# Kernel optimization log

Measured on AMD Instinct MI355X. Metric: run time of the kernel, lower is better.

Reference implementation:

```python
import jax, jax.numpy as jnp
import numpy as np

Y, Z, H, R = 32, 64, 256, 256  # y_dim, z_dim, h_dim, rnn_dim
T, B = 200, 2048


def setup_inputs() -> dict:
    key = jax.random.key(0)
    ks = jax.random.split(key, 32)
    w = lambda k, shape: jax.random.normal(k, shape, jnp.float32) * 0.05
    z32 = lambda n: jnp.zeros((n,), jnp.float32)
    return {
        "states": jax.random.normal(ks[0], (T, B, Y), jnp.float32),
        "eps": jax.random.normal(ks[1], (T - 1, B, Z), jnp.float32),
        # encoder q(z|x,y,h): Linear(2Y+R,H) ReLU Linear(H,H) ReLU
        "enc_w1": w(ks[2], (H, 2 * Y + R)), "enc_b1": z32(H),
        "enc_w2": w(ks[3], (H, H)), "enc_b2": z32(H),
        "enc_mw": w(ks[4], (Z, H)), "enc_mb": z32(Z),
        "enc_sw": w(ks[5], (Z, H)), "enc_sb": z32(Z),
        # prior p(z|y,h): Linear(Y+R,H) ReLU Linear(H,H) ReLU
        "pri_w1": w(ks[6], (H, Y + R)), "pri_b1": z32(H),
        "pri_w2": w(ks[7], (H, H)), "pri_b2": z32(H),
        "pri_mw": w(ks[8], (Z, H)), "pri_mb": z32(Z),
        "pri_sw": w(ks[9], (Z, H)), "pri_sb": z32(Z),
        # decoder p(x|y,z,h): Linear(Y+Z+R,H) ReLU Linear(H,H) ReLU
        "dec_w1": w(ks[10], (H, Y + Z + R)), "dec_b1": z32(H),
        "dec_w2": w(ks[11], (H, H)), "dec_b2": z32(H),
        "dec_mw": w(ks[12], (Y, H)), "dec_mb": z32(Y),
        "dec_sw": w(ks[13], (Y, H)), "dec_sb": z32(Y),
        # GRU(Y+Z -> R), 1 layer; torch gate order [r, z, n]
        "gru_wih": w(ks[14], (3 * R, Y + Z)), "gru_whh": w(ks[15], (3 * R, R)),
        "gru_bih": z32(3 * R), "gru_bhh": z32(3 * R),
    }


def reference(states, eps, enc_w1, enc_b1, enc_w2, enc_b2, enc_mw, enc_mb,
              enc_sw, enc_sb, pri_w1, pri_b1, pri_w2, pri_b2, pri_mw, pri_mb,
              pri_sw, pri_sb, dec_w1, dec_b1, dec_w2, dec_b2, dec_mw, dec_mb,
              dec_sw, dec_sb, gru_wih, gru_whh, gru_bih, gru_bhh):
    batch = states.shape[1]
    rnn_dim = gru_whh.shape[1]
    relu, sp = jax.nn.relu, jax.nn.softplus
    LOG2PI = jnp.float32(np.log(2.0 * np.pi))

    def mlp2(x, w1, b1, w2, b2):
        return relu(relu(x @ w1.T + b1) @ w2.T + b2)

    def step(h, inp):
        y, x, e = inp  # y=states[t], x=states[t+1], e: reparam noise
        enc_h = mlp2(jnp.concatenate([x, y, h], 1), enc_w1, enc_b1, enc_w2, enc_b2)
        em = enc_h @ enc_mw.T + enc_mb
        es = sp(enc_h @ enc_sw.T + enc_sb)
        pri_h = mlp2(jnp.concatenate([y, h], 1), pri_w1, pri_b1, pri_w2, pri_b2)
        pm = pri_h @ pri_mw.T + pri_mb
        ps = sp(pri_h @ pri_sw.T + pri_sb)
        z = em + es * e  # sample_gauss
        dec_h = mlp2(jnp.concatenate([y, z, h], 1), dec_w1, dec_b1, dec_w2, dec_b2)
        dm = dec_h @ dec_mw.T + dec_mb
        ds = sp(dec_h @ dec_sw.T + dec_sb)
        # GRU cell (torch gate order r,z,n)
        gi = jnp.concatenate([x, z], 1) @ gru_wih.T + gru_bih
        gh = h @ gru_whh.T + gru_bhh
        ir, iz, inn = jnp.split(gi, 3, axis=1)
        hr, hz, hn = jnp.split(gh, 3, axis=1)
        r = jax.nn.sigmoid(ir + hr)
        u = jax.nn.sigmoid(iz + hz)
        n = jnp.tanh(inn + r * hn)
        h_new = (1.0 - u) * n + u * h
        kl = 0.5 * jnp.sum(2.0 * jnp.log(ps / es) + (es ** 2 + (em - pm) ** 2) / ps ** 2 - 1.0)
        nll = jnp.sum(jnp.log(ds) + (x - dm) ** 2 / (2.0 * ds ** 2) + 0.5 * LOG2PI)
        return h_new, (kl, nll)

    h0 = jnp.zeros((batch, rnn_dim), states.dtype)
    _, (kls, nlls) = jax.lax.scan(step, h0, (states[:-1], states[1:], eps))
    # out = [kl_loss, recon_loss]
    return jnp.stack([jnp.sum(kls), jnp.sum(nlls)])
```

## Files before the change

### kernel.cpp

```cpp
#include <hip/hip_runtime.h>

typedef unsigned short u16;
typedef unsigned int u32;
typedef __bf16 bf16x8 __attribute__((ext_vector_type(8)));
typedef float f32x4 __attribute__((ext_vector_type(4)));

#define YD 32
#define ZD 64
#define HD 256
#define RD 256
#define TSTEPS 199
#define BB 2048
#define MROWS 32
#define NBLK 64
#define NTHR 1024
#define CATS 392
#define HBS  264
#define HES  136
#define HDS  72

enum : int {
  OFF_ENC_W1 = 0,
  OFF_ENC_W2 = 81920,
  OFF_ENC_H  = 147456,
  OFF_PRI_W1 = 180224,
  OFF_PRI_W2 = 253952,
  OFF_PRI_H  = 319488,
  OFF_DEC_W1 = 352256,
  OFF_DEC_W2 = 442368,
  OFF_DEC_H  = 507904,
  OFF_GWIH   = 524288,
  OFF_GWHH   = 598016,
};

__device__ __forceinline__ u16 f2bf(float f) {
  u32 u = __float_as_uint(f);
  u += 0x7fffu + ((u >> 16) & 1u);
  return (u16)(u >> 16);
}
__device__ __forceinline__ float bf2f(u16 b) {
  return __uint_as_float((u32)b << 16);
}
__device__ __forceinline__ float softplus_f(float x) {
  float l = __logf(1.f + __expf(-fabsf(x)));
  return x > 0.f ? x + l : l;
}
__device__ __forceinline__ float sigmoid_f(float x) {
  return __builtin_amdgcn_rcpf(1.f + __expf(-x));
}
__device__ __forceinline__ float tanh_f(float x) {
  float e = __expf(-2.f * fabsf(x));
  float t = (1.f - e) * __builtin_amdgcn_rcpf(1.f + e);
  return x >= 0.f ? t : -t;
}

template<int NT, int RT, int KS, int AS>
__device__ __forceinline__ void gemm_seg(f32x4 (&acc)[NT][RT],
    const u16* __restrict__ W, const int Kw, const int wrow0, const int wk0,
    const u16* A, const int acol0, const int rt0, const int lane)
{
  const int n = lane & 15, quad = lane >> 4;
  bf16x8 b[KS][NT];
  #pragma unroll
  for (int nt = 0; nt < NT; ++nt) {
    const u16* wp = W + (size_t)(wrow0 + nt * 16 + n) * Kw + wk0 + quad * 8;
    #pragma unroll
    for (int ks = 0; ks < KS; ++ks)
      b[ks][nt] = *reinterpret_cast<const bf16x8*>(wp + ks * 32);
  }
  #pragma unroll
  for (int ks = 0; ks < KS; ++ks) {
    bf16x8 a[RT];
    #pragma unroll
    for (int rt = 0; rt < RT; ++rt)
      a[rt] = *reinterpret_cast<const bf16x8*>(A + ((rt0 + rt) * 16 + n) * AS + acol0 + ks * 32 + quad * 8);
    #pragma unroll
    for (int nt = 0; nt < NT; ++nt)
      #pragma unroll
      for (int rt = 0; rt < RT; ++rt)
        acc[nt][rt] = __builtin_amdgcn_mfma_f32_16x16x32_bf16(a[rt], b[ks][nt], acc[nt][rt], 0, 0, 0);
  }
}

template<int RT, int DS>
__device__ __forceinline__ void store_relu(const f32x4 (&acc)[1][RT], u16* dst,
    const int col0, const int rt0, const float bias, const int lane)
{
  const int n = lane & 15, quad = lane >> 4;
  #pragma unroll
  for (int rt = 0; rt < RT; ++rt)
    #pragma unroll
    for (int i = 0; i < 4; ++i) {
      float v = fmaxf(acc[0][rt][i] + bias, 0.f);
      dst[((rt0 + rt) * 16 + quad * 4 + i) * DS + col0 + n] = f2bf(v);
    }
}

struct PrepArgs { const float* src[14]; int off[14]; int cnt[14]; };

__global__ void prep_weights(PrepArgs a, u16* __restrict__ dst) {
  const int j = blockIdx.y;
  const float* __restrict__ s = a.src[j];
  u16* d = dst + a.off[j];
  const int nel = a.cnt[j];
  for (int i = blockIdx.x * blockDim.x + threadIdx.x; i < nel; i += gridDim.x * blockDim.x)
    d[i] = f2bf(s[i]);
}

__global__ void zero_out_k(float* out) { if (threadIdx.x < 2) out[threadIdx.x] = 0.f; }

__global__ __launch_bounds__(NTHR, 4)
void vrnn_kernel(const float* __restrict__ states, const float* __restrict__ eps,
                 const float* __restrict__ enc_b1, const float* __restrict__ enc_b2,
                 const float* __restrict__ enc_mb, const float* __restrict__ enc_sb,
                 const float* __restrict__ pri_b1, const float* __restrict__ pri_b2,
                 const float* __restrict__ pri_mb, const float* __restrict__ pri_sb,
                 const float* __restrict__ dec_b1, const float* __restrict__ dec_b2,
                 const float* __restrict__ dec_mb, const float* __restrict__ dec_sb,
                 const float* __restrict__ gbih, const float* __restrict__ gbhh,
                 const u16* __restrict__ ws, float* __restrict__ out)
{
  __shared__ u16 cat[MROWS * CATS];
  __shared__ u16 hb1[MROWS * HBS];
  __shared__ u16 hb2[MROWS * HBS];
  __shared__ u16 hbhE[MROWS * HES];
  __shared__ u16 hbhP[MROWS * HES];
  __shared__ u16 hbhD[MROWS * HDS];

  const int tid = threadIdx.x;
  const int w = tid >> 6, lane = tid & 63;
  const int n = lane & 15, quad = lane >> 4;
  const int r0 = blockIdx.x * MROWS;
  const int n0 = w * 16;
  const int cgE = w & 7, rtE = w >> 3;
  const int cgD = w & 3, rtD = (w >> 2) & 1;

  const int jW = n0 + n;
  const float b1e = enc_b1[jW], b2e = enc_b2[jW];
  const float b1p = pri_b1[jW], b2p = pri_b2[jW];
  const float b1d = dec_b1[jW], b2d = dec_b2[jW];
  const float brg = gbih[jW] + gbhh[jW];
  const float bug = gbih[RD + jW] + gbhh[RD + jW];
  const float bing = gbih[2 * RD + jW];
  const float bhng = gbhh[2 * RD + jW];
  const float bhE = (cgE < 4) ? enc_mb[cgE * 16 + n] : enc_sb[(cgE - 4) * 16 + n];
  const float bhP = (cgE < 4) ? pri_mb[cgE * 16 + n] : pri_sb[(cgE - 4) * 16 + n];
  const float bhD = (cgD < 2) ? dec_mb[cgD * 16 + n] : dec_sb[(cgD - 2) * 16 + n];

  for (int i = tid; i < MROWS * (HD / 2); i += NTHR) {
    int row = i >> 7, c = (i & 127) * 2;
    *reinterpret_cast<u32*>(&cat[row * CATS + 128 + c]) = 0u;
  }

  float hreg[2][4];
  #pragma unroll
  for (int a = 0; a < 2; ++a)
    #pragma unroll
    for (int c = 0; c < 4; ++c) hreg[a][c] = 0.f;

  const int srow = (tid & 255) >> 3, sc4 = (tid & 7) * 4;
  float4 xyf = make_float4(0.f, 0.f, 0.f, 0.f);
  if (tid < 512)
    xyf = *reinterpret_cast<const float4*>(states + ((size_t)((tid < 256) ? 1 : 0) * BB + r0 + srow) * YD + sc4);

  const int mz = tid >> 5, jz = (tid & 31) * 2;
  const int mn = (tid & 511) >> 4, jn = (tid & 15) * 2;

  float kl_acc = 0.f, nll_acc = 0.f;

  for (int t = 0; t < TSTEPS; ++t) {
    if (tid < 512) {
      u16* d = cat + srow * CATS + ((tid < 256) ? 0 : 32) + sc4;
      d[0] = f2bf(xyf.x); d[1] = f2bf(xyf.y); d[2] = f2bf(xyf.z); d[3] = f2bf(xyf.w);
    }
    float2 ev2 = *reinterpret_cast<const float2*>(eps + ((size_t)t * BB + r0 + mz) * ZD + jz);
    float2 xs2 = make_float2(0.f, 0.f);
    if (tid < 512)
      xs2 = *reinterpret_cast<const float2*>(states + ((size_t)(t + 1) * BB + r0 + mn) * YD + jn);
    __syncthreads();

    {
      f32x4 acc[1][2] = {};
      gemm_seg<1, 2, 2, CATS>(acc, ws + OFF_ENC_W1, 320, n0, 0, cat, 0, 0, lane);
      gemm_seg<1, 2, 8, CATS>(acc, ws + OFF_ENC_W1, 320, n0, 64, cat, 128, 0, lane);
      store_relu<2, HBS>(acc, hb1, n0, 0, b1e, lane);
    }
    __syncthreads();

    {
      f32x4 acc[1][2] = {};
      gemm_seg<1, 2, 8, HBS>(acc, ws + OFF_ENC_W2, 256, n0, 0, hb1, 0, 0, lane);
      store_relu<2, HBS>(acc, hb2, n0, 0, b2e, lane);
    }
    __syncthreads();

    {
      f32x4 acc[1][1] = {};
      gemm_seg<1, 1, 8, HBS>(acc, ws + OFF_ENC_H, 256, cgE * 16, 0, hb2, 0, rtE, lane);
      #pragma unroll
      for (int i = 0; i < 4; ++i) {
        float v = acc[0][0][i] + bhE;
        if (cgE >= 4) v = softplus_f(v);
        hbhE[(rtE * 16 + quad * 4 + i) * HES + cgE * 16 + n] = f2bf(v);
      }
    }
    __syncthreads();

    {
      float em0 = bf2f(hbhE[mz * HES + jz]);
      float em1 = bf2f(hbhE[mz * HES + jz + 1]);
      float es0 = bf2f(hbhE[mz * HES + 64 + jz]);
      float es1 = bf2f(hbhE[mz * HES + 64 + jz + 1]);
      cat[mz * CATS + 64 + jz] = f2bf(em0 + es0 * ev2.x);
      cat[mz * CATS + 64 + jz + 1] = f2bf(em1 + es1 * ev2.y);
      f32x4 acc[1][2] = {};
      gemm_seg<1, 2, 1, CATS>(acc, ws + OFF_PRI_W1, 288, n0, 0, cat, 32, 0, lane);
      gemm_seg<1, 2, 8, CATS>(acc, ws + OFF_PRI_W1, 288, n0, 32, cat, 128, 0, lane);
      store_relu<2, HBS>(acc, hb1, n0, 0, b1p, lane);
    }
    __syncthreads();

    {
      f32x4 acc[1][2] = {};
      gemm_seg<1, 2, 8, HBS>(acc, ws + OFF_PRI_W2, 256, n0, 0, hb1, 0, 0, lane);
      store_relu<2, HBS>(acc, hb2, n0, 0, b2p, lane);
    }
    __syncthreads();

    {
      f32x4 acc[1][1] = {};
      gemm_seg<1, 1, 8, HBS>(acc, ws + OFF_PRI_H, 256, cgE * 16, 0, hb2, 0, rtE, lane);
      #pragma unroll
      for (int i = 0; i < 4; ++i) {
        float v = acc[0][0][i] + bhP;
        if (cgE >= 4) v = softplus_f(v);
        hbhP[(rtE * 16 + quad * 4 + i) * HES + cgE * 16 + n] = f2bf(v);
      }
    }
    __syncthreads();

    {
      #pragma unroll
      for (int c = 0; c < 2; ++c) {
        float em = bf2f(hbhE[mz * HES + jz + c]);
        float es = bf2f(hbhE[mz * HES + 64 + jz + c]);
        float pm = bf2f(hbhP[mz * HES + jz + c]);
        float ps = bf2f(hbhP[mz * HES + 64 + jz + c]);
        float d = em - pm;
        kl_acc += 0.5f * (2.f * __logf(ps * __builtin_amdgcn_rcpf(es))
                          + (es * es + d * d) / (ps * ps) - 1.f);
      }
      f32x4 acc[1][2] = {};
      gemm_seg<1, 2, 3, CATS>(acc, ws + OFF_DEC_W1, 352, n0, 0, cat, 32, 0, lane);
      gemm_seg<1, 2, 8, CATS>(acc, ws + OFF_DEC_W1, 352, n0, 96, cat, 128, 0, lane);
      store_relu<2, HBS>(acc, hb1, n0, 0, b1d, lane);
    }
    __syncthreads();

    {
      f32x4 acc[1][2] = {};
      gemm_seg<1, 2, 8, HBS>(acc, ws + OFF_DEC_W2, 256, n0, 0, hb1, 0, 0, lane);
      store_relu<2, HBS>(acc, hb2, n0, 0, b2d, lane);
    }
    __syncthreads();

    {
      if (w < 8) {
        f32x4 acc[1][1] = {};
        gemm_seg<1, 1, 8, HBS>(acc, ws + OFF_DEC_H, 256, cgD * 16, 0, hb2, 0, rtD, lane);
        #pragma unroll
        for (int i = 0; i < 4; ++i) {
          float v = acc[0][0][i] + bhD;
          if (cgD >= 2) v = softplus_f(v);
          hbhD[(rtD * 16 + quad * 4 + i) * HDS + cgD * 16 + n] = f2bf(v);
        }
      }
      f32x4 aH[1][2] = {};
      gemm_seg<1, 2, 8, CATS>(aH, ws + OFF_GWHH, 256, 2 * RD + n0, 0, cat, 128, 0, lane);
      {
        f32x4 aR[1][2] = {};
        gemm_seg<1, 2, 1, CATS>(aR, ws + OFF_GWIH, 96, n0, 0, cat, 0, 0, lane);
        gemm_seg<1, 2, 2, CATS>(aR, ws + OFF_GWIH, 96, n0, 32, cat, 64, 0, lane);
        gemm_seg<1, 2, 8, CATS>(aR, ws + OFF_GWHH, 256, n0, 0, cat, 128, 0, lane);
        #pragma unroll
        for (int rt = 0; rt < 2; ++rt)
          #pragma unroll
          for (int i = 0; i < 4; ++i)
            aH[0][rt][i] = sigmoid_f(aR[0][rt][i] + brg) * (aH[0][rt][i] + bhng);
      }
      {
        f32x4 aN[1][2] = {};
        gemm_seg<1, 2, 1, CATS>(aN, ws + OFF_GWIH, 96, 2 * RD + n0, 0, cat, 0, 0, lane);
        gemm_seg<1, 2, 2, CATS>(aN, ws + OFF_GWIH, 96, 2 * RD + n0, 32, cat, 64, 0, lane);
        #pragma unroll
        for (int rt = 0; rt < 2; ++rt)
          #pragma unroll
          for (int i = 0; i < 4; ++i)
            aH[0][rt][i] = tanh_f(aN[0][rt][i] + bing + aH[0][rt][i]);
      }
      {
        f32x4 aU[1][2] = {};
        gemm_seg<1, 2, 1, CATS>(aU, ws + OFF_GWIH, 96, RD + n0, 0, cat, 0, 0, lane);
        gemm_seg<1, 2, 2, CATS>(aU, ws + OFF_GWIH, 96, RD + n0, 32, cat, 64, 0, lane);
        gemm_seg<1, 2, 8, CATS>(aU, ws + OFF_GWHH, 256, RD + n0, 0, cat, 128, 0, lane);
        #pragma unroll
        for (int rt = 0; rt < 2; ++rt)
          #pragma unroll
          for (int i = 0; i < 4; ++i) {
            float u = sigmoid_f(aU[0][rt][i] + bug);
            hreg[rt][i] = (1.f - u) * aH[0][rt][i] + u * hreg[rt][i];
          }
      }
      const int tn = (t + 1 < TSTEPS) ? t + 1 : TSTEPS - 1;
      if (tid < 512)
        xyf = *reinterpret_cast<const float4*>(states + ((size_t)((tid < 256) ? tn + 1 : tn) * BB + r0 + srow) * YD + sc4);
    }
    __syncthreads();

    if (tid < 512) {
      #pragma unroll
      for (int c = 0; c < 2; ++c) {
        float dm = bf2f(hbhD[mn * HDS + jn + c]);
        float ds = bf2f(hbhD[mn * HDS + 32 + jn + c]);
        float xv = (c == 0) ? xs2.x : xs2.y;
        float dd = xv - dm;
        nll_acc += __logf(ds) + dd * dd / (2.f * ds * ds) + 0.91893853320467274178f;
      }
    }
    #pragma unroll
    for (int rt = 0; rt < 2; ++rt)
      #pragma unroll
      for (int i = 0; i < 4; ++i)
        cat[(rt * 16 + quad * 4 + i) * CATS + 128 + n0 + n] = f2bf(hreg[rt][i]);
  }

  float kv = kl_acc, nv = nll_acc;
  #pragma unroll
  for (int off = 32; off > 0; off >>= 1) {
    kv += __shfl_down(kv, off, 64);
    nv += __shfl_down(nv, off, 64);
  }
  if (lane == 0) {
    atomicAdd(out + 0, kv);
    atomicAdd(out + 1, nv);
  }
}

extern "C" void kernel_launch(void* const* d_in, const int* in_sizes, int n_in,
                              void* d_out, int out_size, void* d_ws, size_t ws_size,
                              hipStream_t stream) {
  const float* states = (const float*)d_in[0];
  const float* eps    = (const float*)d_in[1];
  u16* ws   = (u16*)d_ws;
  float* out = (float*)d_out;

  PrepArgs pa;
  const int jsrc[14] = {2, 4, 6, 8, 10, 12, 14, 16, 18, 20, 22, 24, 26, 27};
  const int joff[14] = {OFF_ENC_W1, OFF_ENC_W2, OFF_ENC_H, OFF_ENC_H + 16384,
                        OFF_PRI_W1, OFF_PRI_W2, OFF_PRI_H, OFF_PRI_H + 16384,
                        OFF_DEC_W1, OFF_DEC_W2, OFF_DEC_H, OFF_DEC_H + 8192,
                        OFF_GWIH, OFF_GWHH};
  const int jcnt[14] = {81920, 65536, 16384, 16384,
                        73728, 65536, 16384, 16384,
                        90112, 65536, 8192, 8192,
                        73728, 196608};
  for (int j = 0; j < 14; ++j) {
    pa.src[j] = (const float*)d_in[jsrc[j]];
    pa.off[j] = joff[j];
    pa.cnt[j] = jcnt[j];
  }

  zero_out_k<<<dim3(1), dim3(64), 0, stream>>>(out);
  prep_weights<<<dim3(64, 14), dim3(256), 0, stream>>>(pa, ws);
  vrnn_kernel<<<dim3(NBLK), dim3(NTHR), 0, stream>>>(
      states, eps,
      (const float*)d_in[3],  (const float*)d_in[5],
      (const float*)d_in[7],  (const float*)d_in[9],
      (const float*)d_in[11], (const float*)d_in[13],
      (const float*)d_in[15], (const float*)d_in[17],
      (const float*)d_in[19], (const float*)d_in[21],
      (const float*)d_in[23], (const float*)d_in[25],
      (const float*)d_in[28], (const float*)d_in[29],
      ws, out);
}
```

Measured before the change: 10.76 ms.

## Software-pipeline VRNN step: run encoder/GRU alongside prior/decoder of previous step

Restructures the per-step schedule so warp groups specialise. Warps 0-7 run the encoder and GRU for step t, warps 8-11 run the prior and warps 12-15 the decoder for step t-1, using double-buffered h, z and encoder-head buffers plus a triple-buffered y ring. This cuts the barriers per step from about ten to four and lets independent branches overlap. The batch tile per block is halved to 16 rows (128 blocks), which gives more blocks but less weight reuse per block, and the staggered index logic across t and t-1 risks off-by-one mistakes.

```diff
diff --git a/kernel.cpp b/kernel.cpp
--- a/kernel.cpp
+++ b/kernel.cpp
@@ -11,13 +11,15 @@
 #define RD 256
 #define TSTEPS 199
 #define BB 2048
-#define MROWS 32
-#define NBLK 64
+#define MROWS 16
+#define NBLK 128
 #define NTHR 1024
-#define CATS 392
-#define HBS  264
-#define HES  136
-#define HDS  72
+#define YS  40
+#define ZS  72
+#define HS  264
+#define HBS 264
+#define HES 136
+#define HDS 72
 
 enum : int {
   OFF_ENC_W1 = 0,
@@ -82,17 +84,17 @@
   }
 }
 
-template<int RT, int DS>
-__device__ __forceinline__ void store_relu(const f32x4 (&acc)[1][RT], u16* dst,
-    const int col0, const int rt0, const float bias, const int lane)
+template<int NT, int DS>
+__device__ __forceinline__ void store_relu_n(const f32x4 (&acc)[NT][1], u16* dst,
+    const int col0, const float (&bias)[NT], const int lane)
 {
   const int n = lane & 15, quad = lane >> 4;
   #pragma unroll
-  for (int rt = 0; rt < RT; ++rt)
+  for (int nt = 0; nt < NT; ++nt)
     #pragma unroll
     for (int i = 0; i < 4; ++i) {
-      float v = fmaxf(acc[0][rt][i] + bias, 0.f);
-      dst[((rt0 + rt) * 16 + quad * 4 + i) * DS + col0 + n] = f2bf(v);
+      float v = fmaxf(acc[nt][0][i] + bias[nt], 0.f);
+      dst[(quad * 4 + i) * DS + col0 + nt * 16 + n] = f2bf(v);
     }
 }
 
@@ -120,218 +122,261 @@
                  const float* __restrict__ gbih, const float* __restrict__ gbhh,
                  const u16* __restrict__ ws, float* __restrict__ out)
 {
-  __shared__ u16 cat[MROWS * CATS];
-  __shared__ u16 hb1[MROWS * HBS];
-  __shared__ u16 hb2[MROWS * HBS];
-  __shared__ u16 hbhE[MROWS * HES];
-  __shared__ u16 hbhP[MROWS * HES];
-  __shared__ u16 hbhD[MROWS * HDS];
+  __shared__ __align__(16) u16 yb[3][MROWS * YS];
+  __shared__ __align__(16) u16 zb[2][MROWS * ZS];
+  __shared__ __align__(16) u16 hbuf[2][MROWS * HS];
+  __shared__ __align__(16) u16 hb1A[MROWS * HBS], hb2A[MROWS * HBS];
+  __shared__ __align__(16) u16 hb1P[MROWS * HBS], hb2P[MROWS * HBS];
+  __shared__ __align__(16) u16 hb1D[MROWS * HBS], hb2D[MROWS * HBS];
+  __shared__ __align__(16) u16 hbhE[2][MROWS * HES];
+  __shared__ __align__(16) u16 hbhP[MROWS * HES];
+  __shared__ __align__(16) u16 hbhD[MROWS * HDS];
 
   const int tid = threadIdx.x;
   const int w = tid >> 6, lane = tid & 63;
   const int n = lane & 15, quad = lane >> 4;
   const int r0 = blockIdx.x * MROWS;
-  const int n0 = w * 16;
-  const int cgE = w & 7, rtE = w >> 3;
-  const int cgD = w & 3, rtD = (w >> 2) & 1;
-
-  const int jW = n0 + n;
-  const float b1e = enc_b1[jW], b2e = enc_b2[jW];
-  const float b1p = pri_b1[jW], b2p = pri_b2[jW];
-  const float b1d = dec_b1[jW], b2d = dec_b2[jW];
-  const float brg = gbih[jW] + gbhh[jW];
-  const float bug = gbih[RD + jW] + gbhh[RD + jW];
-  const float bing = gbih[2 * RD + jW];
-  const float bhng = gbhh[2 * RD + jW];
-  const float bhE = (cgE < 4) ? enc_mb[cgE * 16 + n] : enc_sb[(cgE - 4) * 16 + n];
-  const float bhP = (cgE < 4) ? pri_mb[cgE * 16 + n] : pri_sb[(cgE - 4) * 16 + n];
-  const float bhD = (cgD < 2) ? dec_mb[cgD * 16 + n] : dec_sb[(cgD - 2) * 16 + n];
+  const int n0A = w * 32;
+
+  float b1e[2] = {}, b2e[2] = {}, brg[2] = {}, bug[2] = {}, bing[2] = {}, bhng[2] = {};
+  float mbE = 0.f, sbE = 0.f;
+  float b1p[4] = {}, b2p[4] = {}, bhP[2] = {};
+  float b1d[4] = {}, b2d[4] = {}, bhD = 0.f;
+  if (w < 8) {
+    #pragma unroll
+    for (int s = 0; s < 2; ++s) {
+      const int c = n0A + s * 16 + n;
+      b1e[s] = enc_b1[c]; b2e[s] = enc_b2[c];
+      brg[s] = gbih[c] + gbhh[c];
+      bug[s] = gbih[RD + c] + gbhh[RD + c];
+      bing[s] = gbih[2 * RD + c];
+      bhng[s] = gbhh[2 * RD + c];
+    }
+    if (w < 4) { mbE = enc_mb[w * 16 + n]; sbE = enc_sb[w * 16 + n]; }
+  } else if (w < 12) {
+    const int p = w - 8;
+    #pragma unroll
+    for (int k = 0; k < 4; ++k) {
+      const int c = p * 64 + k * 16 + n;
+      b1p[k] = pri_b1[c]; b2p[k] = pri_b2[c];
+    }
+    #pragma unroll
+    for (int k = 0; k < 2; ++k) {
+      const int r = p * 32 + k * 16 + n;
+      bhP[k] = (r < 64) ? pri_mb[r] : pri_sb[r - 64];
+    }
+  } else {
+    const int d_ = w - 12;
+    #pragma unroll
+    for (int k = 0; k < 4; ++k) {
+      const int c = d_ * 64 + k * 16 + n;
+      b1d[k] = dec_b1[c]; b2d[k] = dec_b2[c];
+    }
+    const int r = d_ * 16 + n;
+    bhD = (r < 32) ? dec_mb[r] : dec_sb[r - 32];
+  }
 
   for (int i = tid; i < MROWS * (HD / 2); i += NTHR) {
     int row = i >> 7, c = (i & 127) * 2;
-    *reinterpret_cast<u32*>(&cat[row * CATS + 128 + c]) = 0u;
-  }
+    *reinterpret_cast<u32*>(&hbuf[0][row * HS + c]) = 0u;
+  }
+  if (tid < 256) {
+    const int row = tid >> 4, c2 = (tid & 15) * 2;
+    float2 a0 = *reinterpret_cast<const float2*>(states + ((size_t)0 * BB + r0 + row) * YD + c2);
+    float2 a1 = *reinterpret_cast<const float2*>(states + ((size_t)1 * BB + r0 + row) * YD + c2);
+    yb[0][row * YS + c2] = f2bf(a0.x); yb[0][row * YS + c2 + 1] = f2bf(a0.y);
+    yb[1][row * YS + c2] = f2bf(a1.x); yb[1][row * YS + c2 + 1] = f2bf(a1.y);
+  }
+  __syncthreads();
 
   float hreg[2][4];
   #pragma unroll
-  for (int a = 0; a < 2; ++a)
-    #pragma unroll
-    for (int c = 0; c < 4; ++c) hreg[a][c] = 0.f;
-
-  const int srow = (tid & 255) >> 3, sc4 = (tid & 7) * 4;
-  float4 xyf = make_float4(0.f, 0.f, 0.f, 0.f);
-  if (tid < 512)
-    xyf = *reinterpret_cast<const float4*>(states + ((size_t)((tid < 256) ? 1 : 0) * BB + r0 + srow) * YD + sc4);
-
-  const int mz = tid >> 5, jz = (tid & 31) * 2;
-  const int mn = (tid & 511) >> 4, jn = (tid & 15) * 2;
+  for (int s = 0; s < 2; ++s)
+    #pragma unroll
+    for (int i = 0; i < 4; ++i) hreg[s][i] = 0.f;
 
   float kl_acc = 0.f, nll_acc = 0.f;
-
-  for (int t = 0; t < TSTEPS; ++t) {
-    if (tid < 512) {
-      u16* d = cat + srow * CATS + ((tid < 256) ? 0 : 32) + sc4;
-      d[0] = f2bf(xyf.x); d[1] = f2bf(xyf.y); d[2] = f2bf(xyf.z); d[3] = f2bf(xyf.w);
-    }
-    float2 ev2 = *reinterpret_cast<const float2*>(eps + ((size_t)t * BB + r0 + mz) * ZD + jz);
-    float2 xs2 = make_float2(0.f, 0.f);
-    if (tid < 512)
-      xs2 = *reinterpret_cast<const float2*>(states + ((size_t)(t + 1) * BB + r0 + mn) * YD + jn);
+  int ym0 = 0, ym1 = 1, ym2 = 2;
+
+  for (int t = 0; t <= TSTEPS; ++t) {
+    const int pa = t & 1, pb = pa ^ 1;
+    f32x4 agh[3][2][1] = {};
+
+    if (w < 8) {
+      if (t < TSTEPS) {
+        f32x4 acc[2][1] = {};
+        gemm_seg<2,1,1,YS>(acc, ws + OFF_ENC_W1, 320, n0A, 0,   yb[ym1], 0, 0, lane);
+        gemm_seg<2,1,1,YS>(acc, ws + OFF_ENC_W1, 320, n0A, 32,  yb[ym0], 0, 0, lane);
+        gemm_seg<2,1,4,HS>(acc, ws + OFF_ENC_W1, 320, n0A, 64,  hbuf[pa], 0,   0, lane);
+        gemm_seg<2,1,4,HS>(acc, ws + OFF_ENC_W1, 320, n0A, 192, hbuf[pa], 128, 0, lane);
+        store_relu_n<2, HBS>(acc, hb1A, n0A, b1e, lane);
+        gemm_seg<2,1,4,HS>(agh[0], ws + OFF_GWHH, 256, n0A, 0,   hbuf[pa], 0,   0, lane);
+        gemm_seg<2,1,4,HS>(agh[0], ws + OFF_GWHH, 256, n0A, 128, hbuf[pa], 128, 0, lane);
+      }
+    } else if (w < 12) {
+      if (t > 0) {
+        const int n0 = (w - 8) * 64;
+        f32x4 acc[4][1] = {};
+        gemm_seg<4,1,1,YS>(acc, ws + OFF_PRI_W1, 288, n0, 0,   yb[ym2], 0, 0, lane);
+        gemm_seg<4,1,4,HS>(acc, ws + OFF_PRI_W1, 288, n0, 32,  hbuf[pb], 0,   0, lane);
+        gemm_seg<4,1,4,HS>(acc, ws + OFF_PRI_W1, 288, n0, 160, hbuf[pb], 128, 0, lane);
+        store_relu_n<4, HBS>(acc, hb1P, n0, b1p, lane);
+      }
+    } else {
+      if (t > 0) {
+        const int n0 = (w - 12) * 64;
+        f32x4 acc[4][1] = {};
+        gemm_seg<4,1,1,YS>(acc, ws + OFF_DEC_W1, 352, n0, 0,   yb[ym2], 0, 0, lane);
+        gemm_seg<4,1,2,ZS>(acc, ws + OFF_DEC_W1, 352, n0, 32,  zb[pb], 0, 0, lane);
+        gemm_seg<4,1,4,HS>(acc, ws + OFF_DEC_W1, 352, n0, 96,  hbuf[pb], 0,   0, lane);
+        gemm_seg<4,1,4,HS>(acc, ws + OFF_DEC_W1, 352, n0, 224, hbuf[pb], 128, 0, lane);
+        store_relu_n<4, HBS>(acc, hb1D, n0, b1d, lane);
+      }
+    }
     __syncthreads();
 
-    {
-      f32x4 acc[1][2] = {};
-      gemm_seg<1, 2, 2, CATS>(acc, ws + OFF_ENC_W1, 320, n0, 0, cat, 0, 0, lane);
-      gemm_seg<1, 2, 8, CATS>(acc, ws + OFF_ENC_W1, 320, n0, 64, cat, 128, 0, lane);
-      store_relu<2, HBS>(acc, hb1, n0, 0, b1e, lane);
+    if (w < 8) {
+      if (t < TSTEPS) {
+        f32x4 acc[2][1] = {};
+        gemm_seg<2,1,4,HBS>(acc, ws + OFF_ENC_W2, 256, n0A, 0,   hb1A, 0,   0, lane);
+        gemm_seg<2,1,4,HBS>(acc, ws + OFF_ENC_W2, 256, n0A, 128, hb1A, 128, 0, lane);
+        store_relu_n<2, HBS>(acc, hb2A, n0A, b2e, lane);
+        #pragma unroll
+        for (int g = 1; g < 3; ++g) {
+          gemm_seg<2,1,4,HS>(agh[g], ws + OFF_GWHH, 256, g * RD + n0A, 0,   hbuf[pa], 0,   0, lane);
+          gemm_seg<2,1,4,HS>(agh[g], ws + OFF_GWHH, 256, g * RD + n0A, 128, hbuf[pa], 128, 0, lane);
+        }
+      }
+    } else if (w < 12) {
+      if (t > 0) {
+        const int n0 = (w - 8) * 64;
+        f32x4 acc[4][1] = {};
+        gemm_seg<4,1,4,HBS>(acc, ws + OFF_PRI_W2, 256, n0, 0,   hb1P, 0,   0, lane);
+        gemm_seg<4,1,4,HBS>(acc, ws + OFF_PRI_W2, 256, n0, 128, hb1P, 128, 0, lane);
+        store_relu_n<4, HBS>(acc, hb2P, n0, b2p, lane);
+      }
+    } else {
+      if (t > 0) {
+        const int n0 = (w - 12) * 64;
+        f32x4 acc[4][1] = {};
+        gemm_seg<4,1,4,HBS>(acc, ws + OFF_DEC_W2, 256, n0, 0,   hb1D, 0,   0, lane);
+        gemm_seg<4,1,4,HBS>(acc, ws + OFF_DEC_W2, 256, n0, 128, hb1D, 128, 0, lane);
+        store_relu_n<4, HBS>(acc, hb2D, n0, b2d, lane);
+      }
     }
     __syncthreads();
 
-    {
-      f32x4 acc[1][2] = {};
-      gemm_seg<1, 2, 8, HBS>(acc, ws + OFF_ENC_W2, 256, n0, 0, hb1, 0, 0, lane);
-      store_relu<2, HBS>(acc, hb2, n0, 0, b2e, lane);
-    }
-    __syncthreads();
-
-    {
-      f32x4 acc[1][1] = {};
-      gemm_seg<1, 1, 8, HBS>(acc, ws + OFF_ENC_H, 256, cgE * 16, 0, hb2, 0, rtE, lane);
-      #pragma unroll
-      for (int i = 0; i < 4; ++i) {
-        float v = acc[0][0][i] + bhE;
-        if (cgE >= 4) v = softplus_f(v);
-        hbhE[(rtE * 16 + quad * 4 + i) * HES + cgE * 16 + n] = f2bf(v);
-      }
-    }
-    __syncthreads();
-
-    {
-      float em0 = bf2f(hbhE[mz * HES + jz]);
-      float em1 = bf2f(hbhE[mz * HES + jz + 1]);
-      float es0 = bf2f(hbhE[mz * HES + 64 + jz]);
-      float es1 = bf2f(hbhE[mz * HES + 64 + jz + 1]);
-      cat[mz * CATS + 64 + jz] = f2bf(em0 + es0 * ev2.x);
-      cat[mz * CATS + 64 + jz + 1] = f2bf(em1 + es1 * ev2.y);
-      f32x4 acc[1][2] = {};
-      gemm_seg<1, 2, 1, CATS>(acc, ws + OFF_PRI_W1, 288, n0, 0, cat, 32, 0, lane);
-      gemm_seg<1, 2, 8, CATS>(acc, ws + OFF_PRI_W1, 288, n0, 32, cat, 128, 0, lane);
-      store_relu<2, HBS>(acc, hb1, n0, 0, b1p, lane);
-    }
-    __syncthreads();
-
-    {
-      f32x4 acc[1][2] = {};
-      gemm_seg<1, 2, 8, HBS>(acc, ws + OFF_PRI_W2, 256, n0, 0, hb1, 0, 0, lane);
-      store_relu<2, HBS>(acc, hb2, n0, 0, b2p, lane);
-    }
-    __syncthreads();
-
-    {
-      f32x4 acc[1][1] = {};
-      gemm_seg<1, 1, 8, HBS>(acc, ws + OFF_PRI_H, 256, cgE * 16, 0, hb2, 0, rtE, lane);
-      #pragma unroll
-      for (int i = 0; i < 4; ++i) {
-        float v = acc[0][0][i] + bhP;
-        if (cgE >= 4) v = softplus_f(v);
-        hbhP[(rtE * 16 + quad * 4 + i) * HES + cgE * 16 + n] = f2bf(v);
-      }
-    }
-    __syncthreads();
-
-    {
-      #pragma unroll
-      for (int c = 0; c < 2; ++c) {
-        float em = bf2f(hbhE[mz * HES + jz + c]);
-        float es = bf2f(hbhE[mz * HES + 64 + jz + c]);
-        float pm = bf2f(hbhP[mz * HES + jz + c]);
-        float ps = bf2f(hbhP[mz * HES + 64 + jz + c]);
-        float d = em - pm;
-        kl_acc += 0.5f * (2.f * __logf(ps * __builtin_amdgcn_rcpf(es))
-                          + (es * es + d * d) / (ps * ps) - 1.f);
-      }
-      f32x4 acc[1][2] = {};
-      gemm_seg<1, 2, 3, CATS>(acc, ws + OFF_DEC_W1, 352, n0, 0, cat, 32, 0, lane);
-      gemm_seg<1, 2, 8, CATS>(acc, ws + OFF_DEC_W1, 352, n0, 96, cat, 128, 0, lane);
-      store_relu<2, HBS>(acc, hb1, n0, 0, b1d, lane);
-    }
-    __syncthreads();
-
-    {
-      f32x4 acc[1][2] = {};
-      gemm_seg<1, 2, 8, HBS>(acc, ws + OFF_DEC_W2, 256, n0, 0, hb1, 0, 0, lane);
-      store_relu<2, HBS>(acc, hb2, n0, 0, b2d, lane);
-    }
-    __syncthreads();
-
-    {
-      if (w < 8) {
+    if (w < 4) {
+      if (t < TSTEPS) {
+        const int c = w * 16 + n;
+        float ev[4];
+        #pragma unroll
+        for (int i = 0; i < 4; ++i)
+          ev[i] = eps[((size_t)t * BB + r0 + quad * 4 + i) * ZD + c];
+        f32x4 am[1][1] = {}, asx[1][1] = {};
+        gemm_seg<1,1,8,HBS>(am,  ws + OFF_ENC_H, 256, w * 16,      0, hb2A, 0, 0, lane);
+        gemm_seg<1,1,8,HBS>(asx, ws + OFF_ENC_H, 256, 64 + w * 16, 0, hb2A, 0, 0, lane);
+        u16* he = hbhE[pa];
+        #pragma unroll
+        for (int i = 0; i < 4; ++i) {
+          const int row = quad * 4 + i;
+          u16 bm = f2bf(am[0][0][i] + mbE);
+          u16 bs = f2bf(softplus_f(asx[0][0][i] + sbE));
+          he[row * HES + c] = bm;
+          he[row * HES + 64 + c] = bs;
+          zb[pa][row * ZS + c] = f2bf(bf2f(bm) + bf2f(bs) * ev[i]);
+        }
+      }
+    } else if (w >= 8 && w < 12) {
+      if (t > 0) {
+        const int p = w - 8, n0 = p * 32;
+        f32x4 acc[2][1] = {};
+        gemm_seg<2,1,8,HBS>(acc, ws + OFF_PRI_H, 256, n0, 0, hb2P, 0, 0, lane);
+        #pragma unroll
+        for (int k = 0; k < 2; ++k)
+          #pragma unroll
+          for (int i = 0; i < 4; ++i) {
+            float v = acc[k][0][i] + bhP[k];
+            if (p >= 2) v = softplus_f(v);
+            hbhP[(quad * 4 + i) * HES + n0 + k * 16 + n] = f2bf(v);
+          }
+      }
+    } else if (w >= 12) {
+      if (t > 0) {
+        const int d_ = w - 12;
         f32x4 acc[1][1] = {};
-        gemm_seg<1, 1, 8, HBS>(acc, ws + OFF_DEC_H, 256, cgD * 16, 0, hb2, 0, rtD, lane);
+        gemm_seg<1,1,8,HBS>(acc, ws + OFF_DEC_H, 256, d_ * 16, 0, hb2D, 0, 0, lane);
         #pragma unroll
         for (int i = 0; i < 4; ++i) {
           float v = acc[0][0][i] + bhD;
-          if (cgD >= 2) v = softplus_f(v);
-          hbhD[(rtD * 16 + quad * 4 + i) * HDS + cgD * 16 + n] = f2bf(v);
-        }
-      }
-      f32x4 aH[1][2] = {};
-      gemm_seg<1, 2, 8, CATS>(aH, ws + OFF_GWHH, 256, 2 * RD + n0, 0, cat, 128, 0, lane);
-      {
-        f32x4 aR[1][2] = {};
-        gemm_seg<1, 2, 1, CATS>(aR, ws + OFF_GWIH, 96, n0, 0, cat, 0, 0, lane);
-        gemm_seg<1, 2, 2, CATS>(aR, ws + OFF_GWIH, 96, n0, 32, cat, 64, 0, lane);
-        gemm_seg<1, 2, 8, CATS>(aR, ws + OFF_GWHH, 256, n0, 0, cat, 128, 0, lane);
-        #pragma unroll
-        for (int rt = 0; rt < 2; ++rt)
-          #pragma unroll
-          for (int i = 0; i < 4; ++i)
-            aH[0][rt][i] = sigmoid_f(aR[0][rt][i] + brg) * (aH[0][rt][i] + bhng);
-      }
-      {
-        f32x4 aN[1][2] = {};
-        gemm_seg<1, 2, 1, CATS>(aN, ws + OFF_GWIH, 96, 2 * RD + n0, 0, cat, 0, 0, lane);
-        gemm_seg<1, 2, 2, CATS>(aN, ws + OFF_GWIH, 96, 2 * RD + n0, 32, cat, 64, 0, lane);
-        #pragma unroll
-        for (int rt = 0; rt < 2; ++rt)
-          #pragma unroll
-          for (int i = 0; i < 4; ++i)
-            aH[0][rt][i] = tanh_f(aN[0][rt][i] + bing + aH[0][rt][i]);
-      }
-      {
-        f32x4 aU[1][2] = {};
-        gemm_seg<1, 2, 1, CATS>(aU, ws + OFF_GWIH, 96, RD + n0, 0, cat, 0, 0, lane);
-        gemm_seg<1, 2, 2, CATS>(aU, ws + OFF_GWIH, 96, RD + n0, 32, cat, 64, 0, lane);
-        gemm_seg<1, 2, 8, CATS>(aU, ws + OFF_GWHH, 256, RD + n0, 0, cat, 128, 0, lane);
-        #pragma unroll
-        for (int rt = 0; rt < 2; ++rt)
+          if (d_ >= 2) v = softplus_f(v);
+          hbhD[(quad * 4 + i) * HDS + d_ * 16 + n] = f2bf(v);
+        }
+      }
+    }
+    __syncthreads();
+
+    if (w < 8) {
+      if (t < TSTEPS) {
+        f32x4 agi[3][2][1] = {};
+        #pragma unroll
+        for (int g = 0; g < 3; ++g) {
+          gemm_seg<2,1,1,YS>(agi[g], ws + OFF_GWIH, 96, g * RD + n0A, 0,  yb[ym1], 0, 0, lane);
+          gemm_seg<2,1,2,ZS>(agi[g], ws + OFF_GWIH, 96, g * RD + n0A, 32, zb[pa],  0, 0, lane);
+        }
+        u16* hn = hbuf[pb];
+        #pragma unroll
+        for (int s = 0; s < 2; ++s)
           #pragma unroll
           for (int i = 0; i < 4; ++i) {
-            float u = sigmoid_f(aU[0][rt][i] + bug);
-            hreg[rt][i] = (1.f - u) * aH[0][rt][i] + u * hreg[rt][i];
+            float r = sigmoid_f(agi[0][s][0][i] + agh[0][s][0][i] + brg[s]);
+            float u = sigmoid_f(agi[1][s][0][i] + agh[1][s][0][i] + bug[s]);
+            float nn = tanh_f(agi[2][s][0][i] + bing[s] + r * (agh[2][s][0][i] + bhng[s]));
+            float hv = (1.f - u) * nn + u * hreg[s][i];
+            hreg[s][i] = hv;
+            hn[(quad * 4 + i) * HS + n0A + s * 16 + n] = f2bf(hv);
           }
       }
-      const int tn = (t + 1 < TSTEPS) ? t + 1 : TSTEPS - 1;
-      if (tid < 512)
-        xyf = *reinterpret_cast<const float4*>(states + ((size_t)((tid < 256) ? tn + 1 : tn) * BB + r0 + srow) * YD + sc4);
+    } else if (w < 12) {
+      const int e = tid - 512;
+      if (t > 0) {
+        const u16* he = hbhE[pb];
+        const int m = e >> 4, j0 = e & 15;
+        #pragma unroll
+        for (int k = 0; k < 4; ++k) {
+          const int j = j0 + k * 16;
+          float em = bf2f(he[m * HES + j]);
+          float es = bf2f(he[m * HES + 64 + j]);
+          float pm = bf2f(hbhP[m * HES + j]);
+          float ps = bf2f(hbhP[m * HES + 64 + j]);
+          float d = em - pm;
+          kl_acc += 0.5f * (2.f * __logf(ps * __builtin_amdgcn_rcpf(es))
+                            + (es * es + d * d) / (ps * ps) - 1.f);
+        }
+      }
+      if (t + 2 <= TSTEPS) {
+        const int row = e >> 4, c2 = (e & 15) * 2;
+        float2 v = *reinterpret_cast<const float2*>(states + ((size_t)(t + 2) * BB + r0 + row) * YD + c2);
+        u16* dd = &yb[ym2][row * YS + c2];
+        dd[0] = f2bf(v.x); dd[1] = f2bf(v.y);
+      }
+    } else {
+      if (t > 0) {
+        const int e = tid - 768, m = e >> 4, j2 = (e & 15) * 2;
+        float2 xv = *reinterpret_cast<const float2*>(states + ((size_t)t * BB + r0 + m) * YD + j2);
+        #pragma unroll
+        for (int c = 0; c < 2; ++c) {
+          float dm = bf2f(hbhD[m * HDS + j2 + c]);
+          float ds = bf2f(hbhD[m * HDS + 32 + j2 + c]);
+          float xf = c ? xv.y : xv.x;
+          float dd = xf - dm;
+          nll_acc += __logf(ds) + dd * dd / (2.f * ds * ds) + 0.91893853320467274178f;
+        }
+      }
     }
     __syncthreads();
 
-    if (tid < 512) {
-      #pragma unroll
-      for (int c = 0; c < 2; ++c) {
-        float dm = bf2f(hbhD[mn * HDS + jn + c]);
-        float ds = bf2f(hbhD[mn * HDS + 32 + jn + c]);
-        float xv = (c == 0) ? xs2.x : xs2.y;
-        float dd = xv - dm;
-        nll_acc += __logf(ds) + dd * dd / (2.f * ds * ds) + 0.91893853320467274178f;
-      }
-    }
-    #pragma unroll
-    for (int rt = 0; rt < 2; ++rt)
-      #pragma unroll
-      for (int i = 0; i < 4; ++i)
-        cat[(rt * 16 + quad * 4 + i) * CATS + 128 + n0 + n] = f2bf(hreg[rt][i]);
+    const int tmp = ym0; ym0 = ym1; ym1 = ym2; ym2 = tmp;
   }
 
   float kv = kl_acc, nv = nll_acc;
```

New measurement: 10.08 ms. -6.4%, faster.
